# Optimization experiments

Hardware: AMD Instinct MI355X
Metric: run time of the kernel (lower is better)

## Reference

```python
import jax, jax.numpy as jnp
import numpy as np

V, D, NS, H, L, B, T = 96, 256, 24, 512, 2, 64, 128
TAU = 1.0


def setup_inputs() -> dict:
    key = jax.random.key(0)
    ks = jax.random.split(key, 20)

    def nrm(k, shape, s=0.02):
        return (jax.random.normal(k, shape, jnp.float32) * s).astype(jnp.float32)

    return {
        "x": jax.random.randint(ks[0], (B, T), 0, V),
        "emb": nrm(ks[1], (V, D)),
        "pos_emb": nrm(ks[2], (1024, D)),
        # per-layer params stacked on leading L axis; Linear weights stored (in, out)
        "route_w1": nrm(ks[3], (L, 2 * D, D)),
        "route_b1": jnp.zeros((L, D), jnp.float32),
        "route_w2": nrm(ks[4], (L, D, NS)),
        "route_b2": jnp.zeros((L, NS), jnp.float32),
        # GRUCell: weight_ih/hh are [3D, D] (r,z,n gate order, torch layout)
        "gru_wih": nrm(ks[5], (L, 3 * D, D), 0.5 / np.sqrt(D)),
        "gru_whh": nrm(ks[6], (L, 3 * D, D), 0.5 / np.sqrt(D)),
        "gru_bih": jnp.zeros((L, 3 * D), jnp.float32),
        "gru_bhh": jnp.zeros((L, 3 * D), jnp.float32),
        "proj_w": nrm(ks[7], (L, D, D)),
        "proj_b": jnp.zeros((L, D), jnp.float32),
        "ln1_g": jnp.ones((L, D), jnp.float32),
        "ln1_b": jnp.zeros((L, D), jnp.float32),
        "ffn_w1": nrm(ks[8], (L, D, H)),
        "ffn_b1": jnp.zeros((L, H), jnp.float32),
        "ffn_w2": nrm(ks[9], (L, H, D)),
        "ffn_b2": jnp.zeros((L, D), jnp.float32),
        "ln2_g": jnp.ones((L, D), jnp.float32),
        "ln2_b": jnp.zeros((L, D), jnp.float32),
        "lnout_g": jnp.ones((D,), jnp.float32),
        "lnout_b": jnp.zeros((D,), jnp.float32),
        "head_w": nrm(ks[10], (D, V)),
        "head_b": jnp.zeros((V,), jnp.float32),
    }


def _layernorm(v, g, b, eps=1e-5):
    m = v.mean(-1, keepdims=True)
    c = v - m
    var = (c * c).mean(-1, keepdims=True)
    return c * jax.lax.rsqrt(var + eps) * g + b


def reference(x, emb, pos_emb, route_w1, route_b1, route_w2, route_b2,
              gru_wih, gru_whh, gru_bih, gru_bhh, proj_w, proj_b,
              ln1_g, ln1_b, ffn_w1, ffn_b1, ffn_w2, ffn_b2, ln2_g, ln2_b,
              lnout_g, lnout_b, head_w, head_b):

    def block(xv, S, i):
        # xv: [B, D], S: [B, NS, D]
        slot_mean = S.mean(axis=1)                                   # [B, D]
        ctx = jnp.concatenate([xv, slot_mean], axis=-1)              # [B, 2D]
        hmid = jax.nn.gelu(ctx @ route_w1[i] + route_b1[i], approximate=False)
        alpha = jax.nn.softmax((hmid @ route_w2[i] + route_b2[i]) / TAU, axis=-1)  # [B, NS]
        U = alpha[..., None] * xv[:, None, :]                        # [B, NS, D]
        # GRUCell on flattened (B*NS) "batch"
        gi = jnp.einsum('bsd,ed->bse', U, gru_wih[i]) + gru_bih[i]   # [B, NS, 3D]
        gh = jnp.einsum('bsd,ed->bse', S, gru_whh[i]) + gru_bhh[i]
        ir, iz, in_ = jnp.split(gi, 3, axis=-1)
        hr, hz, hn = jnp.split(gh, 3, axis=-1)
        r = jax.nn.sigmoid(ir + hr)
        z = jax.nn.sigmoid(iz + hz)
        n = jnp.tanh(in_ + r * hn)
        S_new = (1.0 - z) * n + z * S                                # [B, NS, D]
        slot_ctx = jnp.einsum('bs,bsd->bd', alpha, S_new)            # [B, D]
        x_mid = xv + slot_ctx @ proj_w[i] + proj_b[i]
        h1 = _layernorm(x_mid, ln1_g[i], ln1_b[i])
        ff = jax.nn.gelu(h1 @ ffn_w1[i] + ffn_b1[i], approximate=False) @ ffn_w2[i] + ffn_b2[i]
        x_out = _layernorm(x_mid + ff, ln2_g[i], ln2_b[i])
        return x_out, S_new

    def step(S_stack, inp):
        tok, p = inp                                                 # tok: [B], p: [D]
        xv = emb[tok] + p
        new_S = []
        for i in range(L):
            xv, Si = block(xv, S_stack[i], i)
            new_S.append(Si)
        logits_t = _layernorm(xv, lnout_g, lnout_b) @ head_w + head_b  # [B, V]
        return jnp.stack(new_S), logits_t

    S0 = jnp.zeros((L, x.shape[0], NS, D), jnp.float32)
    _, logits = jax.lax.scan(step, S0, (x.T, pos_emb[:x.shape[1]]))  # logits: [T, B, V]
    return jnp.transpose(logits, (1, 0, 2))                          # [B, T, V]
```

## Files before the change

### kernel.cpp

```cpp
#include <hip/hip_runtime.h>
#include <hip/hip_fp16.h>

typedef unsigned short u16;
typedef _Float16 f16x8 __attribute__((ext_vector_type(8)));
typedef float f32x4 __attribute__((ext_vector_type(4)));

#define VV   96
#define DD   256
#define NSL  24
#define HH   512
#define LL   2
#define BB   64
#define TT   128

#define EXB    3489792u
#define SBYT   45056u
#define OF_R2P 0u
#define OF_PJP 1024u
#define OF_F2P 9216u
#define OF_SM  17408u
#define OF_S16 19456u
#define OF_FLAGS (EXB + 64u*SBYT)

#define AG_ST(p,v) __hip_atomic_store((p),(v),__ATOMIC_RELAXED,__HIP_MEMORY_SCOPE_AGENT)
#define AG_LD(p)   __hip_atomic_load((p),__ATOMIC_RELAXED,__HIP_MEMORY_SCOPE_AGENT)

__device__ __forceinline__ u16 f2h(float f){ return __half_as_ushort(__float2half(f)); }
__device__ __forceinline__ float gelu_f(float x){ return 0.5f*x*(1.f+erff(x*0.70710678118654752f)); }
__device__ __forceinline__ float sigm_f(float x){ return 1.f/(1.f+__expf(-x)); }
__device__ __forceinline__ float tanh_f(float x){
  x = fminf(15.f, fmaxf(-15.f, x));
  float e2 = __expf(2.f*x);
  return (e2-1.f)/(e2+1.f);
}

__device__ __forceinline__ float dotg8(const u16* __restrict__ row, const float* __restrict__ v,
                                       int g, int iters){
  float acc = 0.f;
  #pragma unroll
  for(int it=0; it<iters; ++it){
    int k = (it*8 + g)*8;
    uint4 w = *(const uint4*)(row + k);
    float4 a  = *(const float4*)(v + k);
    float4 bq = *(const float4*)(v + k + 4);
    float2 f0 = __half22float2(*(const __half2*)&w.x);
    float2 f1 = __half22float2(*(const __half2*)&w.y);
    float2 f2_ = __half22float2(*(const __half2*)&w.z);
    float2 f3 = __half22float2(*(const __half2*)&w.w);
    acc += f0.x*a.x + f0.y*a.y + f1.x*a.z + f1.y*a.w;
    acc += f2_.x*bq.x + f2_.y*bq.y + f3.x*bq.z + f3.y*bq.w;
  }
  return acc;
}
__device__ __forceinline__ float dotg16(const u16* __restrict__ row, const float* __restrict__ v,
                                        int tl, int iters){
  float acc = 0.f;
  #pragma unroll
  for(int it=0; it<iters; ++it){
    int k = (it*16 + tl)*8;
    uint4 w = *(const uint4*)(row + k);
    float4 a  = *(const float4*)(v + k);
    float4 bq = *(const float4*)(v + k + 4);
    float2 f0 = __half22float2(*(const __half2*)&w.x);
    float2 f1 = __half22float2(*(const __half2*)&w.y);
    float2 f2_ = __half22float2(*(const __half2*)&w.z);
    float2 f3 = __half22float2(*(const __half2*)&w.w);
    acc += f0.x*a.x + f0.y*a.y + f1.x*a.z + f1.y*a.w;
    acc += f2_.x*bq.x + f2_.y*bq.y + f3.x*bq.z + f3.y*bq.w;
  }
  return acc;
}
__device__ __forceinline__ float red8(float a){
  a += __shfl_down(a,4,64); a += __shfl_down(a,2,64); a += __shfl_down(a,1,64);
  return a;
}
__device__ __forceinline__ float red16(float a){
  a += __shfl_down(a,8,64); a += __shfl_down(a,4,64);
  a += __shfl_down(a,2,64); a += __shfl_down(a,1,64);
  return a;
}

__device__ __forceinline__ void syncq(unsigned* flags, int b, int c, unsigned ep, int tid){
  __syncthreads();
  if(tid==0){
    AG_ST(&flags[b*4+c], ep);
    const int p0=(c+1)&3, p1=(c+2)&3, p2=(c+3)&3;
    for(;;){
      unsigned a0 = AG_LD(&flags[b*4+p0]);
      unsigned a1 = AG_LD(&flags[b*4+p1]);
      unsigned a2 = AG_LD(&flags[b*4+p2]);
      if(a0>=ep && a1>=ep && a2>=ep) break;
      __builtin_amdgcn_s_sleep(2);
    }
  }
  __syncthreads();
}
__device__ __forceinline__ void syncq_arrive(unsigned* flags, int b, int c, unsigned ep, int tid){
  __syncthreads();
  if(tid==0) AG_ST(&flags[b*4+c], ep);
}
__device__ __forceinline__ void syncq_wait(unsigned* flags, int b, int c, unsigned ep, int tid){
  if(tid==0){
    const int p0=(c+1)&3, p1=(c+2)&3, p2=(c+3)&3;
    for(;;){
      unsigned a0 = AG_LD(&flags[b*4+p0]);
      unsigned a1 = AG_LD(&flags[b*4+p1]);
      unsigned a2 = AG_LD(&flags[b*4+p2]);
      if(a0>=ep && a1>=ep && a2>=ep) break;
      __builtin_amdgcn_s_sleep(2);
    }
  }
  __syncthreads();
}

__global__ void k_cvt(const float* __restrict__ s, u16* __restrict__ d, int n){
  int i = blockIdx.x*256 + threadIdx.x;
  if(i<n) d[i] = f2h(s[i]);
}
__global__ void k_cvtT(const float* __restrict__ s, u16* __restrict__ d, int K, int N){
  int i = blockIdx.x*256 + threadIdx.x;
  if(i < K*N){ int k = i/N, n = i - k*N; d[n*K + k] = f2h(s[i]); }
}
__global__ void k_zeroflags(unsigned* f){ f[threadIdx.x] = 0u; }

__global__ __launch_bounds__(1024, 4) void ssr_main(
    const int* __restrict__ x, const float* __restrict__ emb, const float* __restrict__ pos,
    const u16* __restrict__ r1T, const float* __restrict__ b_r1,
    const u16* __restrict__ r2T, const float* __restrict__ b_r2,
    const u16* __restrict__ wihW, const u16* __restrict__ whhW,
    const float* __restrict__ bih, const float* __restrict__ bhh,
    const u16* __restrict__ pjT, const float* __restrict__ b_pj,
    const float* __restrict__ g1, const float* __restrict__ be1,
    const u16* __restrict__ f1T, const float* __restrict__ b_f1,
    const u16* __restrict__ f2T, const float* __restrict__ b_f2,
    const float* __restrict__ g2, const float* __restrict__ be2,
    const float* __restrict__ go, const float* __restrict__ bo,
    const u16* __restrict__ hdT, const float* __restrict__ b_hd,
    void* __restrict__ wsraw,
    float* __restrict__ out)
{
  extern __shared__ float sm[];
  float* S_l   = sm;
  u16*  sbf    = (u16*)(sm + 3072);
  float* gh_l  = sm + 7296;
  float* gx_l  = sm + 12096;
  float* ctx   = sm + 12288;
  float* xv    = sm + 12800;
  float* xm    = sm + 13056;
  float* h1    = sm + 13312;
  float* hmid_l= sm + 13568;
  float* ff_l  = sm + 13632;
  float* sctx  = sm + 13760;
  float* alpha = sm + 13824;
  float* red   = sm + 13856;
  float* pc    = sm + 13920;

  const int wgid = blockIdx.x;
  const int b = wgid & 63;
  const int c = wgid >> 6;
  const int tid = threadIdx.x;
  const int g = tid & 7,  gid = tid >> 3;
  const int tl = tid & 15, tm = tid >> 4;

  char* exb = (char*)wsraw + EXB + (size_t)b*SBYT;
  float*    ex_r2p = (float*)(exb + OF_R2P);
  float*    ex_pjp = (float*)(exb + OF_PJP);
  float*    ex_f2p = (float*)(exb + OF_F2P);
  float*    ex_sm  = (float*)(exb + OF_SM);
  unsigned* ex_s16 = (unsigned*)(exb + OF_S16);
  unsigned* flags  = (unsigned*)((char*)wsraw + OF_FLAGS);
  unsigned ep = 0;

  for(int i=tid;i<3072;i+=1024) S_l[i]=0.f;
  for(int i=tid;i<4224;i+=1024) ((float*)sbf)[i]=0.f;
  __syncthreads();

  for(int t=0;t<TT;++t){
    const int tok = x[b*TT + t];
    if(tid<DD) xv[tid] = emb[tok*DD+tid] + pos[t*DD+tid];
    __syncthreads();

    for(int li=0; li<LL; ++li){
      if(t>0){
        for(int i=tid;i<3072;i+=1024){
          int s_=i>>7, dw=i&127;
          unsigned d32 = AG_LD(&ex_s16[li*3072+i]);
          *(unsigned*)(sbf + s_*264 + dw*2) = d32;
        }
        if(tid<DD) ctx[DD+tid] = AG_LD(&ex_sm[li*DD+tid]);
      } else {
        if(tid<DD) ctx[DD+tid] = 0.f;
      }
      if(tid<DD) ctx[tid] = xv[tid];
      __syncthreads();

      {
        const u16* row = r1T + (size_t)(li*DD + c*64 + tm)*(2*DD);
        float a = red16(dotg16(row, ctx, tl, 4));
        if(!tl) hmid_l[tm] = gelu_f(a + b_r1[li*DD + c*64 + tm]);
      }
      __syncthreads();
      if(gid < NSL){
        const u16* row = r2T + (size_t)(li*NSL + gid)*DD + c*64;
        float a = red8(dotg8(row, hmid_l, g, 1));
        if(!g) AG_ST(&ex_r2p[li*96 + c*24 + gid], a);
      }
      ++ep;
      syncq_arrive(flags, b, c, ep, tid);
      {
        const u16* W = wihW + (size_t)li*3*DD*DD;
        for(int le=gid; le<192; le+=128){
          int e = (le>>6)*DD + c*64 + (le&63);
          float a = red8(dotg8(W + (size_t)e*DD, xv, g, 4));
          if(!g) gx_l[le] = a;
        }
      }
      {
        const int lane = tid & 63, w = tid >> 6;
        if(w < 12){
          const int lr = lane & 15, lk = lane >> 4;
          const int q = w >> 2, j = w & 3;
          const u16* WB = whhW + (size_t)li*3*DD*DD;
          const u16* a0p = sbf + lr*264 + lk*8;
          const u16* a1p = sbf + (16+lr)*264 + lk*8;
          const u16* bp = WB + (size_t)(q*DD + c*64 + j*16 + lr)*DD + lk*8;
          f32x4 acc0 = {0.f,0.f,0.f,0.f}, acc1 = {0.f,0.f,0.f,0.f};
          #pragma unroll
          for(int ks=0; ks<8; ++ks){
            f16x8 bfr = *(const f16x8*)(bp + ks*32);
            f16x8 a0  = *(const f16x8*)(a0p + ks*32);
            f16x8 a1  = *(const f16x8*)(a1p + ks*32);
            acc0 = __builtin_amdgcn_mfma_f32_16x16x32_f16(a0, bfr, acc0, 0,0,0);
            acc1 = __builtin_amdgcn_mfma_f32_16x16x32_f16(a1, bfr, acc1, 0,0,0);
          }
          int le = q*64 + j*16 + lr;
          #pragma unroll
          for(int r=0;r<4;++r){
            int s0 = lk*4 + r;
            gh_l[s0*200 + le] = acc0[r];
            int s1 = 16 + lk*4 + r;
            if(s1 < NSL) gh_l[s1*200 + le] = acc1[r];
          }
        }
      }
      syncq_wait(flags, b, c, ep, tid);
      if(tid < 32){
        float lg = -1e30f;
        if(tid < NSL){
          lg = b_r2[li*NSL+tid];
          #pragma unroll
          for(int cc=0;cc<4;++cc) lg += AG_LD(&ex_r2p[li*96 + cc*24 + tid]);
        }
        float m = lg;
        #pragma unroll
        for(int o=16;o>0;o>>=1) m = fmaxf(m, __shfl_xor(m,o,32));
        float e = (tid<NSL) ? __expf(lg-m) : 0.f;
        float s = e;
        #pragma unroll
        for(int o=16;o>0;o>>=1) s += __shfl_xor(s,o,32);
        if(tid<NSL) alpha[tid] = e/s;
      }
      __syncthreads();
      {
        int dd = tid & 63, sg = tid >> 6;
        int dg = li*3*DD + c*64 + dd;
        float gir = gx_l[dd],      bir = bih[dg],        bhr = bhh[dg];
        float giz = gx_l[64+dd],   biz = bih[dg+DD],     bhz = bhh[dg+DD];
        float gin = gx_l[128+dd],  bin = bih[dg+2*DD],   bhn = bhh[dg+2*DD];
        float pctx = 0.f;
        float* Sll = S_l + li*NSL*64;
        #pragma unroll
        for(int h=0;h<2;++h){
          int s_ = sg + h*16;
          if(s_ < NSL){
            float al = alpha[s_];
            float hr = gh_l[s_*200 + dd]       + bhr;
            float hz = gh_l[s_*200 + 64 + dd]  + bhz;
            float hn = gh_l[s_*200 + 128 + dd] + bhn;
            float rr = sigm_f(al*gir + bir + hr);
            float zz = sigm_f(al*giz + biz + hz);
            float nn = tanh_f(al*gin + bin + rr*hn);
            float sv = Sll[s_*64+dd];
            float ns = (1.f-zz)*nn + zz*sv;
            Sll[s_*64+dd] = ns;
            pctx += al*ns;
          }
        }
        pc[tid] = pctx;
      }
      __syncthreads();
      if(tid<64){
        float s_=0.f;
        #pragma unroll
        for(int k=0;k<16;++k) s_ += pc[k*64+tid];
        sctx[tid] = s_;
        float m_=0.f;
        const float* Sll = S_l + li*NSL*64;
        #pragma unroll
        for(int s2=0;s2<NSL;++s2) m_ += Sll[s2*64+tid];
        AG_ST(&ex_sm[li*DD + c*64 + tid], m_*(1.f/NSL));
      }
      __syncthreads();
      for(int i=tid;i<768;i+=1024){
        int s_ = i>>5, dp = (i&31)*2;
        const float* Sll = S_l + li*NSL*64;
        unsigned lo = (unsigned)f2h(Sll[s_*64+dp]);
        unsigned hi = (unsigned)f2h(Sll[s_*64+dp+1]);
        AG_ST(&ex_s16[li*3072 + s_*128 + c*32 + (i&31)], lo | (hi<<16));
      }
      {
        #pragma unroll
        for(int p=0;p<2;++p){
          int dout = p*128 + gid;
          const u16* row = pjT + (size_t)(li*DD + dout)*DD + c*64;
          float a = red8(dotg8(row, sctx, g, 1));
          if(!g) AG_ST(&ex_pjp[li*1024 + c*256 + dout], a);
        }
      }
      syncq(flags, b, c, ++ep, tid);
      {
        float v = 0.f;
        if(tid<DD){
          float s_ = b_pj[li*DD+tid];
          #pragma unroll
          for(int cc=0;cc<4;++cc) s_ += AG_LD(&ex_pjp[li*1024 + cc*256 + tid]);
          v = xv[tid] + s_;
          xm[tid] = v;
        }
        float s1 = (tid<DD)?v:0.f, s2 = (tid<DD)?v*v:0.f;
        #pragma unroll
        for(int o=32;o>0;o>>=1){ s1 += __shfl_xor(s1,o,64); s2 += __shfl_xor(s2,o,64); }
        if(tid<DD && (tid&63)==0){ red[tid>>6]=s1; red[8+(tid>>6)]=s2; }
        __syncthreads();
        if(tid<DD){
          float a = red[0]+red[1]+red[2]+red[3];
          float cs= red[8]+red[9]+red[10]+red[11];
          float m = a*(1.f/DD), rs = rsqrtf(cs*(1.f/DD) - m*m + 1e-5f);
          h1[tid] = (v-m)*rs*g1[li*DD+tid] + be1[li*DD+tid];
        }
        __syncthreads();
      }
      if(gid < 128){
        const u16* row = f1T + (size_t)(li*HH + c*128 + gid)*DD;
        float a = red8(dotg8(row, h1, g, 4));
        if(!g) ff_l[gid] = gelu_f(a + b_f1[li*HH + c*128 + gid]);
      }
      __syncthreads();
      {
        #pragma unroll
        for(int p=0;p<4;++p){
          int dout = p*64 + tm;
          const u16* row = f2T + (size_t)(li*DD + dout)*HH + c*128;
          float a = red16(dotg16(row, ff_l, tl, 1));
          if(!tl) AG_ST(&ex_f2p[li*1024 + c*256 + dout], a);
        }
      }
      syncq(flags, b, c, ++ep, tid);
      {
        float v = 0.f;
        if(tid<DD){
          float s_ = b_f2[li*DD+tid];
          #pragma unroll
          for(int cc=0;cc<4;++cc) s_ += AG_LD(&ex_f2p[li*1024 + cc*256 + tid]);
          v = xm[tid] + s_;
        }
        float s1 = (tid<DD)?v:0.f, s2 = (tid<DD)?v*v:0.f;
        #pragma unroll
        for(int o=32;o>0;o>>=1){ s1 += __shfl_xor(s1,o,64); s2 += __shfl_xor(s2,o,64); }
        if(tid<DD && (tid&63)==0){ red[tid>>6]=s1; red[8+(tid>>6)]=s2; }
        __syncthreads();
        if(tid<DD){
          float a = red[0]+red[1]+red[2]+red[3];
          float cs= red[8]+red[9]+red[10]+red[11];
          float m = a*(1.f/DD), rs = rsqrtf(cs*(1.f/DD) - m*m + 1e-5f);
          xv[tid] = (v-m)*rs*g2[li*DD+tid] + be2[li*DD+tid];
        }
        __syncthreads();
      }
    }

    {
      float v = (tid<DD) ? xv[tid] : 0.f;
      float s1 = v, s2 = v*v;
      #pragma unroll
      for(int o=32;o>0;o>>=1){ s1 += __shfl_xor(s1,o,64); s2 += __shfl_xor(s2,o,64); }
      if(tid<DD && (tid&63)==0){ red[tid>>6]=s1; red[8+(tid>>6)]=s2; }
      __syncthreads();
      if(tid<DD){
        float a = red[0]+red[1]+red[2]+red[3];
        float cs= red[8]+red[9]+red[10]+red[11];
        float m = a*(1.f/DD), rs = rsqrtf(cs*(1.f/DD) - m*m + 1e-5f);
        h1[tid] = (v-m)*rs*go[tid] + bo[tid];
      }
      __syncthreads();
    }
    if(gid < NSL){
      int n = c*24 + gid;
      float acc = red8(dotg8(hdT + (size_t)n*DD, h1, g, 4));
      if(!g) out[((size_t)b*TT + t)*VV + n] = acc + b_hd[n];
    }
    __syncthreads();
  }
}

extern "C" void kernel_launch(void* const* d_in, const int* in_sizes, int n_in,
                              void* d_out, int out_size, void* d_ws, size_t ws_size,
                              hipStream_t stream){
  const int*   x    = (const int*)  d_in[0];
  const float* emb  = (const float*)d_in[1];
  const float* pos  = (const float*)d_in[2];
  const float* r1   = (const float*)d_in[3];
  const float* br1  = (const float*)d_in[4];
  const float* r2   = (const float*)d_in[5];
  const float* br2  = (const float*)d_in[6];
  const float* wih  = (const float*)d_in[7];
  const float* whh  = (const float*)d_in[8];
  const float* bih  = (const float*)d_in[9];
  const float* bhh  = (const float*)d_in[10];
  const float* pj   = (const float*)d_in[11];
  const float* bpj  = (const float*)d_in[12];
  const float* g1   = (const float*)d_in[13];
  const float* be1  = (const float*)d_in[14];
  const float* f1   = (const float*)d_in[15];
  const float* bf1  = (const float*)d_in[16];
  const float* f2   = (const float*)d_in[17];
  const float* bf2  = (const float*)d_in[18];
  const float* g2   = (const float*)d_in[19];
  const float* be2  = (const float*)d_in[20];
  const float* go   = (const float*)d_in[21];
  const float* bo   = (const float*)d_in[22];
  const float* hd   = (const float*)d_in[23];
  const float* bhd  = (const float*)d_in[24];
  float* out = (float*)d_out;
  u16* ws = (u16*)d_ws;

  u16* r1T  = ws + 0;
  u16* r2T  = ws + 262144;
  u16* wihW = ws + 274432;
  u16* whhW = ws + 667648;
  u16* pjT  = ws + 1060864;
  u16* f1T  = ws + 1191936;
  u16* f2T  = ws + 1454080;
  u16* hdT  = ws + 1716224;

  k_cvt<<<(2*768*256+255)/256,256,0,stream>>>(wih, wihW, 2*768*256);
  k_cvt<<<(2*768*256+255)/256,256,0,stream>>>(whh, whhW, 2*768*256);
  for(int li=0; li<2; ++li){
    k_cvtT<<<(512*256+255)/256,256,0,stream>>>(r1 + li*512*256, r1T + li*256*512, 512, 256);
    k_cvtT<<<(256*24+255)/256, 256,0,stream>>>(r2 + li*256*24,  r2T + li*24*256,  256, 24);
    k_cvtT<<<(256*256+255)/256,256,0,stream>>>(pj + li*256*256, pjT + li*256*256, 256, 256);
    k_cvtT<<<(256*512+255)/256,256,0,stream>>>(f1 + li*256*512, f1T + li*512*256, 256, 512);
    k_cvtT<<<(512*256+255)/256,256,0,stream>>>(f2 + li*512*256, f2T + li*256*512, 512, 256);
  }
  k_cvtT<<<(256*96+255)/256,256,0,stream>>>(hd, hdT, 256, 96);
  k_zeroflags<<<1,256,0,stream>>>((unsigned*)((char*)d_ws + OF_FLAGS));

  const int smem = 14944*4;
  hipFuncSetAttribute(reinterpret_cast<const void*>(ssr_main),
                      hipFuncAttributeMaxDynamicSharedMemorySize, smem);
  ssr_main<<<4*BB, 1024, smem, stream>>>(x, emb, pos, r1T, br1, r2T, br2, wihW, whhW, bih, bhh,
                                         pjT, bpj, g1, be1, f1T, bf1, f2T, bf2, g2, be2, go, bo,
                                         hdT, bhd, d_ws, out);
}
```

Before: 4.954 ms.

## Double-buffer per-layer slot state loads and prefetch FFN weights across syncs

The fp16 slot states and slot means for each layer now live in separate LDS buffers. The exchange loads for the other layer are moved to run after the routing and GRU-hidden phase, which takes them off the critical path at the start of each layer and removes a barrier. FFN1 weight rows are prefetched into registers between the split arrive and wait of the cross-workgroup sync, so the global load latency overlaps the wait. The cost is more LDS (about 77KB per workgroup) and extra registers held across the sync.

```diff
diff --git a/kernel.cpp b/kernel.cpp
--- a/kernel.cpp
+++ b/kernel.cpp
@@ -141,19 +141,20 @@
 {
   extern __shared__ float sm[];
   float* S_l   = sm;
-  u16*  sbf    = (u16*)(sm + 3072);
-  float* gh_l  = sm + 7296;
-  float* gx_l  = sm + 12096;
-  float* ctx   = sm + 12288;
-  float* xv    = sm + 12800;
-  float* xm    = sm + 13056;
-  float* h1    = sm + 13312;
-  float* hmid_l= sm + 13568;
-  float* ff_l  = sm + 13632;
-  float* sctx  = sm + 13760;
-  float* alpha = sm + 13824;
-  float* red   = sm + 13856;
-  float* pc    = sm + 13920;
+  u16*  sbf0   = (u16*)(sm + 3072);
+  u16*  sbf1   = (u16*)(sm + 7296);
+  float* gh_l  = sm + 11520;
+  float* gx_l  = sm + 16320;
+  float* xv    = sm + 16512;
+  float* smean = sm + 16768;
+  float* xm    = sm + 17280;
+  float* h1    = sm + 17536;
+  float* hmid_l= sm + 17792;
+  float* ff_l  = sm + 17856;
+  float* sctx  = sm + 17984;
+  float* alpha = sm + 18048;
+  float* red   = sm + 18080;
+  float* pc    = sm + 18144;
 
   const int wgid = blockIdx.x;
   const int b = wgid & 63;
@@ -171,8 +172,7 @@
   unsigned* flags  = (unsigned*)((char*)wsraw + OF_FLAGS);
   unsigned ep = 0;
 
-  for(int i=tid;i<3072;i+=1024) S_l[i]=0.f;
-  for(int i=tid;i<4224;i+=1024) ((float*)sbf)[i]=0.f;
+  for(int i=tid;i<19168;i+=1024) sm[i]=0.f;
   __syncthreads();
 
   for(int t=0;t<TT;++t){
@@ -181,22 +181,13 @@
     __syncthreads();
 
     for(int li=0; li<LL; ++li){
-      if(t>0){
-        for(int i=tid;i<3072;i+=1024){
-          int s_=i>>7, dw=i&127;
-          unsigned d32 = AG_LD(&ex_s16[li*3072+i]);
-          *(unsigned*)(sbf + s_*264 + dw*2) = d32;
-        }
-        if(tid<DD) ctx[DD+tid] = AG_LD(&ex_sm[li*DD+tid]);
-      } else {
-        if(tid<DD) ctx[DD+tid] = 0.f;
-      }
-      if(tid<DD) ctx[tid] = xv[tid];
-      __syncthreads();
+      u16* sbf = li ? sbf1 : sbf0;
+      const float* smeanL = smean + li*DD;
 
       {
         const u16* row = r1T + (size_t)(li*DD + c*64 + tm)*(2*DD);
-        float a = red16(dotg16(row, ctx, tl, 4));
+        float a = dotg16(row, xv, tl, 2) + dotg16(row + 256, smeanL, tl, 2);
+        a = red16(a);
         if(!tl) hmid_l[tm] = gelu_f(a + b_r1[li*DD + c*64 + tm]);
       }
       __syncthreads();
@@ -243,6 +234,23 @@
           }
         }
       }
+      if(li==0){
+        if(t>0){
+          for(int i=tid;i<3072;i+=1024){
+            int s_=i>>7, dw=i&127;
+            unsigned d32 = AG_LD(&ex_s16[3072+i]);
+            *(unsigned*)(sbf1 + s_*264 + dw*2) = d32;
+          }
+          if(tid<DD) smean[DD+tid] = AG_LD(&ex_sm[DD+tid]);
+        }
+      } else {
+        for(int i=tid;i<3072;i+=1024){
+          int s_=i>>7, dw=i&127;
+          unsigned d32 = AG_LD(&ex_s16[i]);
+          *(unsigned*)(sbf0 + s_*264 + dw*2) = d32;
+        }
+        if(tid<DD) smean[tid] = AG_LD(&ex_sm[tid]);
+      }
       syncq_wait(flags, b, c, ep, tid);
       if(tid < 32){
         float lg = -1e30f;
@@ -317,7 +325,15 @@
           if(!g) AG_ST(&ex_pjp[li*1024 + c*256 + dout], a);
         }
       }
-      syncq(flags, b, c, ++ep, tid);
+      ++ep;
+      syncq_arrive(flags, b, c, ep, tid);
+      uint4 wf[4];
+      if(gid < 128){
+        const u16* frow = f1T + (size_t)(li*HH + c*128 + gid)*DD;
+        #pragma unroll
+        for(int it=0;it<4;++it) wf[it] = *(const uint4*)(frow + (it*8+g)*8);
+      }
+      syncq_wait(flags, b, c, ep, tid);
       {
         float v = 0.f;
         if(tid<DD){
@@ -341,9 +357,21 @@
         __syncthreads();
       }
       if(gid < 128){
-        const u16* row = f1T + (size_t)(li*HH + c*128 + gid)*DD;
-        float a = red8(dotg8(row, h1, g, 4));
-        if(!g) ff_l[gid] = gelu_f(a + b_f1[li*HH + c*128 + gid]);
+        float acc = 0.f;
+        #pragma unroll
+        for(int it=0;it<4;++it){
+          int k = (it*8+g)*8;
+          float4 a4 = *(const float4*)(h1 + k);
+          float4 b4 = *(const float4*)(h1 + k + 4);
+          float2 f0 = __half22float2(*(const __half2*)&wf[it].x);
+          float2 f1v = __half22float2(*(const __half2*)&wf[it].y);
+          float2 f2v = __half22float2(*(const __half2*)&wf[it].z);
+          float2 f3v = __half22float2(*(const __half2*)&wf[it].w);
+          acc += f0.x*a4.x + f0.y*a4.y + f1v.x*a4.z + f1v.y*a4.w;
+          acc += f2v.x*b4.x + f2v.y*b4.y + f3v.x*b4.z + f3v.y*b4.w;
+        }
+        acc = red8(acc);
+        if(!g) ff_l[gid] = gelu_f(acc + b_f1[li*HH + c*128 + gid]);
       }
       __syncthreads();
       {
@@ -455,7 +483,7 @@
   k_cvtT<<<(256*96+255)/256,256,0,stream>>>(hd, hdT, 256, 96);
   k_zeroflags<<<1,256,0,stream>>>((unsigned*)((char*)d_ws + OF_FLAGS));
 
-  const int smem = 14944*4;
+  const int smem = 19168*4;
   hipFuncSetAttribute(reinterpret_cast<const void*>(ssr_main),
                       hipFuncAttributeMaxDynamicSharedMemorySize, smem);
   ssr_main<<<4*BB, 1024, smem, stream>>>(x, emb, pos, r1T, br1, r2T, br2, wihW, whhW, bih, bhh,
```

Result: slower. 5.306 ms (+7.1%).
